# Kernel optimization log

Measured on AMD Instinct MI355X. Metric: run time of the kernel, lower is better.

## Reference

```python
import jax, jax.numpy as jnp
import numpy as np


def setup_inputs() -> dict:
    key = jax.random.key(0)
    k1, k2, k3, k4 = jax.random.split(key, 4)
    H = W = 1024
    B = 16
    image = jax.random.normal(k1, (1, H, W), dtype=jnp.float32)
    x = jax.random.normal(k2, (B, 1, H, W), dtype=jnp.float32)
    # Conv2d(1, 9, 3) parameters, torch layout: weight (out=9, in=1, 3, 3), bias (9,)
    fan_in = 1 * 3 * 3
    bound = 1.0 / np.sqrt(fan_in)
    W_KL = jax.random.uniform(k3, (9, 1, 3, 3), jnp.float32, -bound, bound)
    b_KL = jax.random.uniform(k4, (9,), jnp.float32, -bound, bound)
    return {"image": image, "x": x, "W_KL": W_KL, "b_KL": b_KL}


def reference(image, x, W_KL, b_KL):
    # K = Conv2d(image): (1,H,W) -> (9,H,W), 'same' padding
    K = jax.lax.conv_general_dilated(
        image[None], W_KL, window_strides=(1, 1), padding='SAME',
        dimension_numbers=('NCHW', 'OIHW', 'NCHW'))[0] + b_KL[:, None, None]
    H, W = image.shape[1], image.shape[2]
    # permute (9,H,W) -> (H,W,9) -> unflatten to per-pixel 3x3 kernels (H,W,3,3)
    K = jnp.transpose(K, (1, 2, 0)).reshape(H, W, 3, 3)
    # Apply spatially-varying 3x3 kernel: y[b,c,h,w] = sum_{a,d} K[h,w,a,d] * x_pad[b,c,h+a,w+d]
    x_pad = jnp.pad(x, ((0, 0), (0, 0), (1, 1), (1, 1)))
    y = jnp.zeros_like(x)
    for a in range(3):
        for d in range(3):
            y = y + K[:, :, a, d] * x_pad[:, :, a:a + H, d:d + W]
    return y
```

## Files before the change

kernel.cpp:

```cpp
#include <hip/hip_runtime.h>

#define IH 1024
#define IW 1024
#define NB 16
#define BPB 4

typedef float v4f __attribute__((ext_vector_type(4)));

__device__ __forceinline__ void load_row6(const float* __restrict__ row, int w0,
                                          int tx, bool valid, float o[6]) {
    if (valid) {
        const v4f m = *(const v4f*)(row + w0);
        float left  = __shfl_up(m.w, 1);
        float right = __shfl_down(m.x, 1);
        if (tx == 0)  left  = (w0 > 0)      ? row[w0 - 1] : 0.f;
        if (tx == 63) right = (w0 + 4 < IW) ? row[w0 + 4] : 0.f;
        o[0] = left; o[1] = m.x; o[2] = m.y; o[3] = m.z; o[4] = m.w; o[5] = right;
    } else {
#pragma unroll
        for (int j = 0; j < 6; ++j) o[j] = 0.f;
    }
}

__global__ __launch_bounds__(512) void fused_smblock(
    const float* __restrict__ image,
    const float* __restrict__ x,
    const float* __restrict__ Wk,
    const float* __restrict__ bk,
    float* __restrict__ out)
{
    const int tx = threadIdx.x;
    const int ty = threadIdx.y;
    const int w0 = blockIdx.x * 256 + tx * 4;
    const int h  = blockIdx.y * 8 + ty;

    float wk[81];
#pragma unroll
    for (int i = 0; i < 81; ++i) wk[i] = Wk[i];
    float bb[9];
#pragma unroll
    for (int c = 0; c < 9; ++c) bb[c] = bk[c];

    float p[3][6];
#pragma unroll
    for (int a = 0; a < 3; ++a) {
        const int hh = h + a - 1;
        load_row6(image + (size_t)(hh < 0 ? 0 : hh) * IW, w0, tx,
                  (hh >= 0 && hh < IH), p[a]);
    }

    float Kv[4][9];
#pragma unroll
    for (int j = 0; j < 4; ++j) {
#pragma unroll
        for (int c = 0; c < 9; ++c) {
            float acc = bb[c];
#pragma unroll
            for (int i = 0; i < 3; ++i)
#pragma unroll
                for (int jj = 0; jj < 3; ++jj)
                    acc = fmaf(wk[c * 9 + i * 3 + jj], p[i][j + jj], acc);
            Kv[j][c] = acc;
        }
    }

    const size_t plane = (size_t)IH * IW;
    const int b0 = blockIdx.z * BPB;
#pragma unroll 2
    for (int bi = 0; bi < BPB; ++bi) {
        const float* xp = x + (size_t)(b0 + bi) * plane;
        float r[3][6];
#pragma unroll
        for (int a = 0; a < 3; ++a) {
            const int hh = h + a - 1;
            load_row6(xp + (size_t)(hh < 0 ? 0 : hh) * IW, w0, tx,
                      (hh >= 0 && hh < IH), r[a]);
        }
        float yv[4];
#pragma unroll
        for (int j = 0; j < 4; ++j) {
            float acc = 0.f;
#pragma unroll
            for (int a = 0; a < 3; ++a)
#pragma unroll
                for (int d = 0; d < 3; ++d)
                    acc = fmaf(Kv[j][a * 3 + d], r[a][j + d], acc);
            yv[j] = acc;
        }
        v4f yvec; yvec.x = yv[0]; yvec.y = yv[1]; yvec.z = yv[2]; yvec.w = yv[3];
        __builtin_nontemporal_store(
            yvec, (v4f*)(out + (size_t)(b0 + bi) * plane + (size_t)h * IW + w0));
    }
}

extern "C" void kernel_launch(void* const* d_in, const int* in_sizes, int n_in,
                              void* d_out, int out_size, void* d_ws, size_t ws_size,
                              hipStream_t stream) {
    const float* image = (const float*)d_in[0];
    const float* x     = (const float*)d_in[1];
    const float* Wk    = (const float*)d_in[2];
    const float* bk    = (const float*)d_in[3];
    float* out = (float*)d_out;

    dim3 block(64, 8);
    dim3 grid(IW / 256, IH / 8, NB / BPB);
    fused_smblock<<<grid, block, 0, stream>>>(image, x, Wk, bk, out);
}
```

Before: 148.0 us.

## Stage input rows through LDS tile instead of per-row global loads with shuffles

```diff
diff --git a/kernel.cpp b/kernel.cpp
--- a/kernel.cpp
+++ b/kernel.cpp
@@ -4,35 +4,57 @@
 #define IW 1024
 #define NB 16
 #define BPB 4
+#define TW 256
+#define TH 4
+#define LROWS 6
+#define LW 272
 
 typedef float v4f __attribute__((ext_vector_type(4)));
 
-__device__ __forceinline__ void load_row6(const float* __restrict__ row, int w0,
-                                          int tx, bool valid, float o[6]) {
-    if (valid) {
-        const v4f m = *(const v4f*)(row + w0);
-        float left  = __shfl_up(m.w, 1);
-        float right = __shfl_down(m.x, 1);
-        if (tx == 0)  left  = (w0 > 0)      ? row[w0 - 1] : 0.f;
-        if (tx == 63) right = (w0 + 4 < IW) ? row[w0 + 4] : 0.f;
-        o[0] = left; o[1] = m.x; o[2] = m.y; o[3] = m.z; o[4] = m.w; o[5] = right;
-    } else {
-#pragma unroll
-        for (int j = 0; j < 6; ++j) o[j] = 0.f;
-    }
-}
-
-__global__ __launch_bounds__(512) void fused_smblock(
+__global__ __launch_bounds__(256) void fused_smblock(
     const float* __restrict__ image,
     const float* __restrict__ x,
     const float* __restrict__ Wk,
     const float* __restrict__ bk,
     float* __restrict__ out)
 {
+    __shared__ float tile[LROWS * LW];
+
     const int tx = threadIdx.x;
     const int ty = threadIdx.y;
-    const int w0 = blockIdx.x * 256 + tx * 4;
-    const int h  = blockIdx.y * 8 + ty;
+    const int W0 = blockIdx.x * TW;
+    const int H0 = blockIdx.y * TH;
+
+    auto stage = [&](const float* __restrict__ plane) {
+#pragma unroll
+        for (int r = ty; r < LROWS; r += TH) {
+            const int hh = H0 - 1 + r;
+            const bool rowok = (hh >= 0) && (hh < IH);
+            const float* rowp = plane + (size_t)(rowok ? hh : 0) * IW;
+#pragma unroll
+            for (int c = tx; c < LW / 4; c += 64) {
+                const int w = W0 - 8 + c * 4;
+                v4f v = {0.f, 0.f, 0.f, 0.f};
+                if (rowok && w >= 0 && w + 3 < IW) {
+                    v = *(const v4f*)(rowp + w);
+                } else if (rowok) {
+                    float* vv = (float*)&v;
+#pragma unroll
+                    for (int j = 0; j < 4; ++j) {
+                        const int wj = w + j;
+                        vv[j] = (wj >= 0 && wj < IW) ? rowp[wj] : 0.f;
+                    }
+                }
+                *(v4f*)&tile[r * LW + c * 4] = v;
+            }
+        }
+    };
+
+    auto window6 = [&](int r, float o[6]) {
+        const float2* base = (const float2*)&tile[r * LW + 4 * tx + 6];
+        const float2 d0 = base[0], d1 = base[1], d2 = base[2], d3 = base[3];
+        o[0] = d0.y; o[1] = d1.x; o[2] = d1.y; o[3] = d2.x; o[4] = d2.y; o[5] = d3.x;
+    };
 
     float wk[81];
 #pragma unroll
@@ -41,41 +63,36 @@
 #pragma unroll
     for (int c = 0; c < 9; ++c) bb[c] = bk[c];
 
-    float p[3][6];
+    stage(image);
+    __syncthreads();
+    float Kv[4][9];
+    {
+        float p[3][6];
 #pragma unroll
-    for (int a = 0; a < 3; ++a) {
-        const int hh = h + a - 1;
-        load_row6(image + (size_t)(hh < 0 ? 0 : hh) * IW, w0, tx,
-                  (hh >= 0 && hh < IH), p[a]);
-    }
-
-    float Kv[4][9];
+        for (int a = 0; a < 3; ++a) window6(ty + a, p[a]);
 #pragma unroll
-    for (int j = 0; j < 4; ++j) {
+        for (int j = 0; j < 4; ++j)
 #pragma unroll
-        for (int c = 0; c < 9; ++c) {
-            float acc = bb[c];
+            for (int c = 0; c < 9; ++c) {
+                float acc = bb[c];
 #pragma unroll
-            for (int i = 0; i < 3; ++i)
+                for (int i = 0; i < 3; ++i)
 #pragma unroll
-                for (int jj = 0; jj < 3; ++jj)
-                    acc = fmaf(wk[c * 9 + i * 3 + jj], p[i][j + jj], acc);
-            Kv[j][c] = acc;
-        }
+                    for (int jj = 0; jj < 3; ++jj)
+                        acc = fmaf(wk[c * 9 + i * 3 + jj], p[i][j + jj], acc);
+                Kv[j][c] = acc;
+            }
     }
 
     const size_t plane = (size_t)IH * IW;
     const int b0 = blockIdx.z * BPB;
-#pragma unroll 2
     for (int bi = 0; bi < BPB; ++bi) {
-        const float* xp = x + (size_t)(b0 + bi) * plane;
-        float r[3][6];
+        __syncthreads();
+        stage(x + (size_t)(b0 + bi) * plane);
+        __syncthreads();
+        float r3[3][6];
 #pragma unroll
-        for (int a = 0; a < 3; ++a) {
-            const int hh = h + a - 1;
-            load_row6(xp + (size_t)(hh < 0 ? 0 : hh) * IW, w0, tx,
-                      (hh >= 0 && hh < IH), r[a]);
-        }
+        for (int a = 0; a < 3; ++a) window6(ty + a, r3[a]);
         float yv[4];
 #pragma unroll
         for (int j = 0; j < 4; ++j) {
@@ -84,12 +101,13 @@
             for (int a = 0; a < 3; ++a)
 #pragma unroll
                 for (int d = 0; d < 3; ++d)
-                    acc = fmaf(Kv[j][a * 3 + d], r[a][j + d], acc);
+                    acc = fmaf(Kv[j][a * 3 + d], r3[a][j + d], acc);
             yv[j] = acc;
         }
         v4f yvec; yvec.x = yv[0]; yvec.y = yv[1]; yvec.z = yv[2]; yvec.w = yv[3];
         __builtin_nontemporal_store(
-            yvec, (v4f*)(out + (size_t)(b0 + bi) * plane + (size_t)h * IW + w0));
+            yvec, (v4f*)(out + (size_t)(b0 + bi) * plane + (size_t)(H0 + ty) * IW
+                         + W0 + 4 * tx));
     }
 }
 
@@ -102,7 +120,7 @@
     const float* bk    = (const float*)d_in[3];
     float* out = (float*)d_out;
 
-    dim3 block(64, 8);
-    dim3 grid(IW / 256, IH / 8, NB / BPB);
+    dim3 block(64, TH);
+    dim3 grid(IW / TW, IH / TH, NB / BPB);
     fused_smblock<<<grid, block, 0, stream>>>(image, x, Wk, bk, out);
 }
```

Measured after the change: 148.9 us. Within noise of the previous version (+0.6%).
